# Kernel optimization log

Hardware: AMD Instinct MI355X
Metric: run time of the kernel (lower is better)

The kernel has to match this reference:

```python
import jax, jax.numpy as jnp
import numpy as np

EPS = 1e-3  # norm_cfg eps
# (kind, stride, padding) per conv; 'subm' = SubMConv3d (same spatial shape, same active mask),
# 'down' = SparseConv3d (strided, mask dilates through the kernel footprint)
_CFGS = [("subm", (1, 1, 1), (1, 1, 1)), ("subm", (1, 1, 1), (1, 1, 1)),
         ("down", (2, 2, 2), (1, 1, 1)), ("subm", (1, 1, 1), (1, 1, 1)),
         ("down", (2, 2, 2), (1, 1, 1)), ("subm", (1, 1, 1), (1, 1, 1)),
         ("down", (2, 2, 2), (1, 1, 0)), ("subm", (1, 1, 1), (1, 1, 1)),
         ("down", (1, 1, 2), (0, 0, 0))]
_WSHAPES = [(16, 16, 3, 3, 3), (16, 16, 3, 3, 3), (32, 16, 3, 3, 3), (32, 32, 3, 3, 3),
            (64, 32, 3, 3, 3), (64, 64, 3, 3, 3), (64, 64, 3, 3, 3), (64, 64, 3, 3, 3),
            (64, 64, 1, 1, 3)]


def _conv3d(x, w, stride, pad):
    return jax.lax.conv_general_dilated(
        x, w, window_strides=stride, padding=[(p, p) for p in pad],
        dimension_numbers=("NCDHW", "OIDHW", "NCDHW"))


def _bn_relu(x, mask, gamma, beta):
    # spconv applies BatchNorm1d to the [n_active, C] feature list, so batch statistics
    # are computed over ACTIVE voxels only; inactive sites stay exactly zero.
    cnt = jnp.maximum(mask.sum(), 1.0)
    mean = (x * mask).sum(axis=(0, 2, 3, 4)) / cnt
    mb = mean[None, :, None, None, None]
    var = (jnp.square(x - mb) * mask).sum(axis=(0, 2, 3, 4)) / cnt
    scale = (gamma * jax.lax.rsqrt(var + EPS))[None, :, None, None, None]
    y = (x - mb) * scale + beta[None, :, None, None, None]
    return jax.nn.relu(y) * mask


def _forward(voxel_features, coors, batch_size, input_shape, ws, gs, bs):
    ss = np.array(list(input_shape)[::-1]) + np.array([0, 0, 1])  # sparse_shape [D,H,W]
    D, H, W = int(ss[0]), int(ss[1]), int(ss[2])
    B, C = int(batch_size), voxel_features.shape[1]
    b, z, y, xi = coors[:, 0], coors[:, 1], coors[:, 2], coors[:, 3]
    # Densify: sparse conv with bias=False on a densified grid computes identical values
    # (inactive inputs are zero); the active-site mask reproduces submanifold masking and
    # the active-only BN statistics.
    x = jnp.zeros((B, C, D, H, W), voxel_features.dtype).at[b, :, z, y, xi].set(voxel_features)
    mask = jnp.zeros((B, 1, D, H, W), voxel_features.dtype).at[b, 0, z, y, xi].set(1.0)
    for (kind, stride, pad), w, g, be in zip(_CFGS, ws, gs, bs):
        x = _conv3d(x, w, stride, pad)
        if kind == "down":
            ones = jnp.ones((1, 1) + w.shape[2:], x.dtype)
            mask = (_conv3d(mask, ones, stride, pad) > 0).astype(x.dtype)
        x = _bn_relu(x, mask, g, be)
    x = x.transpose(0, 1, 4, 2, 3)  # [N, C, W, D, H]
    N, C2, Wd, Dd, Hd = x.shape
    return x.reshape(N, C2 * Wd, Dd, Hd)


def setup_inputs():
    rng = np.random.default_rng(0)
    D, H, W, n_vox, c_in = 40, 200, 200, 60000, 16
    lin = rng.choice(D * H * W, size=n_vox, replace=False)  # unique voxel coords
    coors = np.stack([np.zeros(n_vox, np.int32), (lin // (H * W)).astype(np.int32),
                      ((lin // W) % H).astype(np.int32), (lin % W).astype(np.int32)], axis=1)
    key = jax.random.key(0)
    keys = jax.random.split(key, 1 + len(_WSHAPES))
    out = {"voxel_features": jax.random.normal(keys[0], (n_vox, c_in), jnp.float32),
           "coors": jnp.asarray(coors), "batch_size": 1, "input_shape": (199, 200, 40)}
    for i, shp in enumerate(_WSHAPES):
        fan_in = shp[1] * shp[2] * shp[3] * shp[4]
        out[f"w{i}"] = jax.random.normal(keys[1 + i], shp, jnp.float32) / np.sqrt(fan_in)
        out[f"g{i}"] = jnp.ones((shp[0],), jnp.float32)
        out[f"b{i}"] = jnp.zeros((shp[0],), jnp.float32)
    return out


def reference(voxel_features, coors, batch_size, input_shape,
              w0, w1, w2, w3, w4, w5, w6, w7, w8,
              g0, g1, g2, g3, g4, g5, g6, g7, g8,
              b0, b1, b2, b3, b4, b5, b6, b7, b8):
    ws = [w0, w1, w2, w3, w4, w5, w6, w7, w8]
    gs = [g0, g1, g2, g3, g4, g5, g6, g7, g8]
    bs = [b0, b1, b2, b3, b4, b5, b6, b7, b8]
    return _forward(voxel_features, coors, batch_size, input_shape, ws, gs, bs)
```

## Files before the change

kernel.cpp:

```cpp
#include <hip/hip_runtime.h>
#include <cstddef>

#define EPSV 0.001f

static inline int idiv(int a, int b){ return (a + b - 1) / b; }
static inline int imin(int a, int b){ return a < b ? a : b; }

typedef __attribute__((ext_vector_type(8))) short short8b;
typedef __attribute__((ext_vector_type(4))) float floatx4;

static __device__ inline unsigned short f2bf(float f) {
  unsigned u = __float_as_uint(f);
  unsigned r = (u + 0x7FFFu + ((u >> 16) & 1u)) >> 16;
  return (unsigned short)r;
}

struct WPtrs { const float* w[9]; };

__global__ __launch_bounds__(256)
void repack_w(WPtrs ws, float* __restrict__ wp) {
  constexpr int off[10] = {0,6912,13824,27648,55296,110592,221184,331776,442368,454656};
  constexpr int COs[9] = {16,16,32,32,64,64,64,64,64};
  constexpr int CIs[9] = {16,16,16,32,32,64,64,64,64};
  constexpr int NTs[9] = {27,27,27,27,27,27,27,27,3};
  int idx = blockIdx.x * blockDim.x + threadIdx.x;
  if (idx >= off[9]) return;
  int L = 0;
  #pragma unroll
  for (int k = 0; k < 9; k++) if (idx >= off[k+1]) L = k + 1;
  int r  = idx - off[L];
  int CO = COs[L], CI = CIs[L], NT = NTs[L];
  int co = r % CO; int t = r / CO; int ci = t % CI; int tap = t / CI;
  wp[idx] = ws.w[L][(co*CI + ci)*NT + tap];
}

__global__ __launch_bounds__(256)
void repack_wq(const float* __restrict__ w6, const float* __restrict__ w7,
               const float* __restrict__ w8, float* __restrict__ wq) {
  constexpr int N6 = 110592, N7 = 110592, N8 = 12288;
  int idx = blockIdx.x * blockDim.x + threadIdx.x;
  if (idx >= N6 + N7 + N8) return;
  const float* src; int r; int NT;
  if (idx < N6)            { src = w6; r = idx;          NT = 27; }
  else if (idx < N6 + N7)  { src = w7; r = idx - N6;     NT = 27; }
  else                     { src = w8; r = idx - N6 - N7; NT = 3; }
  int j = r & 3; int co = (r >> 2) & 63; int chunk = (r >> 8) & 15; int tap = r >> 12;
  int ci = chunk*4 + j;
  wq[idx] = src[(co*64 + ci)*NT + tap];
}

__global__ __launch_bounds__(256)
void repack_w3b(const float* __restrict__ w3, unsigned short* __restrict__ wq3) {
  int idx = blockIdx.x * blockDim.x + threadIdx.x;
  if (idx >= 27648) return;
  int ci = idx % 32; int t = idx / 32; int co = t % 32; int tap = t / 32;
  wq3[idx] = f2bf(w3[(co*32 + ci)*27 + tap]);
}

__global__ __launch_bounds__(256)
void scatter_grid(const int* __restrict__ coors, int* __restrict__ grid, int n) {
  int i = blockIdx.x * blockDim.x + threadIdx.x;
  if (i >= n) return;
  int z = coors[4*i+1], y = coors[4*i+2], x = coors[4*i+3];
  grid[(z*200 + y)*200 + x] = i;
}

__global__ __launch_bounds__(256)
void subm16(const float* __restrict__ fin, float* __restrict__ fout,
            const int* __restrict__ coors, const int* __restrict__ grid,
            const float* __restrict__ wp, int n) {
  int i = blockIdx.x * blockDim.x + threadIdx.x;
  if (i >= n) return;
  int z = coors[4*i+1], y = coors[4*i+2], x = coors[4*i+3];
  float acc[16];
  #pragma unroll
  for (int c = 0; c < 16; c++) acc[c] = 0.f;
  for (int kz = 0; kz < 3; kz++) {
    int iz = z + kz - 1; if ((unsigned)iz >= 40u) continue;
    for (int ky = 0; ky < 3; ky++) {
      int iy = y + ky - 1; if ((unsigned)iy >= 200u) continue;
      for (int kx = 0; kx < 3; kx++) {
        int ix = x + kx - 1; if ((unsigned)ix >= 200u) continue;
        int j = grid[(iz*200 + iy)*200 + ix];
        if (j < 0) continue;
        int tap = (kz*3 + ky)*3 + kx;
        const float* fj = fin + (size_t)j*16;
        const float* wb = wp + tap*16*16;
        #pragma unroll
        for (int cq = 0; cq < 4; cq++) {
          float4 av = *reinterpret_cast<const float4*>(fj + cq*4);
          float aj[4] = {av.x, av.y, av.z, av.w};
          #pragma unroll
          for (int j4 = 0; j4 < 4; j4++) {
            #pragma unroll
            for (int c = 0; c < 16; c++) acc[c] += aj[j4] * wb[(cq*4+j4)*16 + c];
          }
        }
      }
    }
  }
  float* o = fout + (size_t)i*16;
  #pragma unroll
  for (int c = 0; c < 16; c++) o[c] = acc[c];
}

__global__ __launch_bounds__(256)
void down16to32(const float* __restrict__ fin, const int* __restrict__ grid,
                float* __restrict__ out, unsigned char* __restrict__ mout,
                const float* __restrict__ wp) {
  constexpr int OD = 20, OH = 100, OW = 100, COPT = 16;
  int vox = blockIdx.x * blockDim.x + threadIdx.x;
  int cog = blockIdx.y;
  if (vox >= OD*OH*OW) return;
  int ox = vox % OW; int t = vox / OW; int oy = t % OH; int oz = t / OH;
  float acc[COPT];
  #pragma unroll
  for (int c = 0; c < COPT; c++) acc[c] = 0.f;
  bool any = false;
  for (int kz = 0; kz < 3; kz++) {
    int iz = oz*2 - 1 + kz; if ((unsigned)iz >= 40u) continue;
    for (int ky = 0; ky < 3; ky++) {
      int iy = oy*2 - 1 + ky; if ((unsigned)iy >= 200u) continue;
      for (int kx = 0; kx < 3; kx++) {
        int ix = ox*2 - 1 + kx; if ((unsigned)ix >= 200u) continue;
        int j = grid[(iz*200 + iy)*200 + ix];
        if (j < 0) continue;
        any = true;
        int tap = (kz*3 + ky)*3 + kx;
        const float* fj = fin + (size_t)j*16;
        const float* wb = wp + (size_t)tap*16*32 + cog*COPT;
        #pragma unroll
        for (int cq = 0; cq < 4; cq++) {
          float4 av = *reinterpret_cast<const float4*>(fj + cq*4);
          float aj[4] = {av.x, av.y, av.z, av.w};
          #pragma unroll
          for (int j4 = 0; j4 < 4; j4++) {
            #pragma unroll
            for (int c = 0; c < COPT; c++) acc[c] += aj[j4] * wb[(cq*4+j4)*32 + c];
          }
        }
      }
    }
  }
  float* o = out + (size_t)vox*32 + cog*COPT;
  #pragma unroll
  for (int c = 0; c < COPT; c++) o[c] = acc[c];
  if (cog == 0) mout[vox] = any ? 1 : 0;
}

__global__ __launch_bounds__(256)
void convm3(const unsigned short* __restrict__ xb, float* __restrict__ out,
            const unsigned short* __restrict__ wq3) {
  constexpr int D = 20, H = 100, W = 100;
  constexpr int LDA = 40;
  __shared__ unsigned short a_lds[64 * LDA];
  __shared__ unsigned short w_lds[32 * LDA];

  const int tid  = threadIdx.x;
  const int lane = tid & 63;
  const int wv   = tid >> 6;
  const int vbase = blockIdx.x * 64;

  const int svox = tid >> 2, sq = tid & 3;
  int gv = vbase + svox;
  int sx = gv % W; int tt = gv / W; int sy = tt % H; int sz = tt / H;

  floatx4 acc0 = {0.f,0.f,0.f,0.f};
  floatx4 acc1 = {0.f,0.f,0.f,0.f};
  const int arow = wv*16 + (lane & 15);
  const int kc   = (lane >> 4) * 8;

  #pragma unroll 1
  for (int tap = 0; tap < 27; tap++) {
    int kz = tap / 9, r9 = tap % 9;
    int ky = r9 / 3, kx = r9 % 3;
    int iz = sz + kz - 1, iy = sy + ky - 1, ix = sx + kx - 1;
    bool ok = ((unsigned)iz < (unsigned)D) & ((unsigned)iy < (unsigned)H)
            & ((unsigned)ix < (unsigned)W);
    float4 av = make_float4(0.f,0.f,0.f,0.f);
    if (ok)
      av = *reinterpret_cast<const float4*>(
          xb + ((size_t)((iz*H + iy)*W + ix)*32 + sq*8));
    __syncthreads();
    *reinterpret_cast<float4*>(&a_lds[svox*LDA + sq*8]) = av;
    if (tid < 128) {
      int co = tid >> 2, h = tid & 3;
      *reinterpret_cast<float4*>(&w_lds[co*LDA + h*8]) =
          *reinterpret_cast<const float4*>(wq3 + ((size_t)(tap*32 + co)*32 + h*8));
    }
    __syncthreads();
    short8b a  = *reinterpret_cast<const short8b*>(&a_lds[arow*LDA + kc]);
    short8b b0 = *reinterpret_cast<const short8b*>(&w_lds[(lane & 15)*LDA + kc]);
    short8b b1 = *reinterpret_cast<const short8b*>(&w_lds[(16 + (lane & 15))*LDA + kc]);
    acc0 = __builtin_amdgcn_mfma_f32_16x16x32_bf16(a, b0, acc0, 0, 0, 0);
    acc1 = __builtin_amdgcn_mfma_f32_16x16x32_bf16(a, b1, acc1, 0, 0, 0);
  }
  int orow = vbase + wv*16 + (lane >> 4) * 4;
  int ocol = lane & 15;
  #pragma unroll
  for (int rr = 0; rr < 4; rr++) {
    out[(size_t)(orow + rr)*32 + ocol]      = acc0[rr];
    out[(size_t)(orow + rr)*32 + 16 + ocol] = acc1[rr];
  }
}

template<int ID,int IH,int IW,int OD,int OH,int OW,int CI,int CO,
         int S,int VX,int CO2,
         int KD,int KH,int KW,int SD,int SH,int SW,int PD,int PH,int PW>
__global__ __launch_bounds__(256)
void convg(const float* __restrict__ in, float* __restrict__ out,
           const float* __restrict__ wp) {
  constexpr int G    = 256 / S;
  static_assert(G * CO2 == CO, "co tiling mismatch");
  constexpr int VT   = S * VX;
  constexpr int NVOX = OD*OH*OW;
  __shared__ float a_lds[VT * CI];
  __shared__ float w_lds[CI * CO];

  const int g   = threadIdx.x % G;
  const int s   = threadIdx.x / G;
  const int co0 = g * CO2;
  const int vbase = blockIdx.x * VT;

  float acc[VX][CO2];
  #pragma unroll
  for (int u = 0; u < VX; u++)
    #pragma unroll
    for (int cc = 0; cc < CO2; cc++) acc[u][cc] = 0.f;

  constexpr int CI4N = CI / 4;
  constexpr int VST  = 256 / CI4N;
  const int sv  = threadIdx.x / CI4N;
  const int sc4 = threadIdx.x % CI4N;

  #pragma unroll 1
  for (int kz = 0; kz < KD; kz++) {
    #pragma unroll 1
    for (int ky = 0; ky < KH; ky++) {
      #pragma unroll 1
      for (int kx = 0; kx < KW; kx++) {
        __syncthreads();
        const float* wt = wp + (size_t)((kz*KH + ky)*KW + kx) * CI * CO;
        #pragma unroll
        for (int i = 0; i < CI*CO/4/256; i++) {
          int idx = threadIdx.x + i*256;
          *reinterpret_cast<float4*>(&w_lds[idx*4]) =
              *reinterpret_cast<const float4*>(wt + idx*4);
        }
        #pragma unroll
        for (int rsub = 0; rsub < VT/VST; rsub++) {
          int vox = rsub*VST + sv;
          int gv  = vbase + vox;
          int vc  = gv < NVOX ? gv : 0;
          int ox = vc % OW; int tt = vc / OW; int oy = tt % OH; int oz = tt / OH;
          int iz = oz*SD - PD + kz;
          int iy = oy*SH - PH + ky;
          int ix = ox*SW - PW + kx;
          bool ok = (gv < NVOX) & ((unsigned)iz < (unsigned)ID)
                  & ((unsigned)iy < (unsigned)IH) & ((unsigned)ix < (unsigned)IW);
          float4 v = make_float4(0.f,0.f,0.f,0.f);
          if (ok) {
            int ipos = (iz*IH + iy)*IW + ix;
            v = *reinterpret_cast<const float4*>(in + (size_t)ipos*CI + sc4*4);
          }
          int dw = vox*CI + ((sc4*4) ^ ((vox & 7) << 2));
          *reinterpret_cast<float4*>(&a_lds[dw]) = v;
        }
        __syncthreads();
        #pragma unroll
        for (int c4 = 0; c4 < CI/4; c4++) {
          float wr[4][CO2];
          #pragma unroll
          for (int jj = 0; jj < 4; jj++)
            #pragma unroll
            for (int q = 0; q < CO2/4; q++) {
              float4 wv = *reinterpret_cast<const float4*>(
                  &w_lds[(c4*4 + jj)*CO + co0 + q*4]);
              wr[jj][q*4+0] = wv.x; wr[jj][q*4+1] = wv.y;
              wr[jj][q*4+2] = wv.z; wr[jj][q*4+3] = wv.w;
            }
          #pragma unroll
          for (int u = 0; u < VX; u++) {
            int r = s + S*u;
            float4 a4 = *reinterpret_cast<const float4*>(
                &a_lds[r*CI + ((c4*4) ^ ((r & 7) << 2))]);
            float av[4] = {a4.x, a4.y, a4.z, a4.w};
            #pragma unroll
            for (int jj = 0; jj < 4; jj++)
              #pragma unroll
              for (int cc = 0; cc < CO2; cc++)
                acc[u][cc] += av[jj] * wr[jj][cc];
          }
        }
      }
    }
  }
  #pragma unroll
  for (int u = 0; u < VX; u++) {
    int gv = vbase + s + S*u;
    if (gv >= NVOX) continue;
    float* o = out + (size_t)gv*CO + co0;
    #pragma unroll
    for (int q = 0; q < CO2/4; q++) {
      float4 v = make_float4(acc[u][q*4+0], acc[u][q*4+1],
                             acc[u][q*4+2], acc[u][q*4+3]);
      *reinterpret_cast<float4*>(o + q*4) = v;
    }
  }
}

template<int ID,int IH,int IW,int OD,int OH,int OW,
         int KD,int KH,int KW,int SD,int SH,int SW,int PD,int PH,int PW>
__global__ __launch_bounds__(256)
void convt(const float* __restrict__ in, float* __restrict__ out,
           const float* __restrict__ wq) {
  constexpr int NT = KD*KH*KW;
  constexpr int NG = (NT + 3) / 4;
  const int v    = blockIdx.x;
  const int lane = threadIdx.x & 63;
  const int q    = threadIdx.x >> 6;
  int ox = v % OW; int t = v / OW; int oy = t % OH; int oz = t / OH;

  __shared__ float a_lds[4][64];
  __shared__ float red[4][64];
  float acc = 0.f;

  #pragma unroll 1
  for (int tg = 0; tg < NG; tg++) {
    int tap = tg*4 + q;
    float val = 0.f;
    if (tap < NT) {
      int kz = tap / (KH*KW); int rr = tap % (KH*KW);
      int ky = rr / KW;       int kx = rr % KW;
      int iz = oz*SD - PD + kz, iy = oy*SH - PH + ky, ix = ox*SW - PW + kx;
      if ((unsigned)iz < (unsigned)ID && (unsigned)iy < (unsigned)IH &&
          (unsigned)ix < (unsigned)IW)
        val = in[(size_t)((iz*IH + iy)*IW + ix)*64 + lane];
    }
    __syncthreads();
    a_lds[q][lane] = val;
    __syncthreads();
    #pragma unroll
    for (int t4 = 0; t4 < 4; t4++) {
      int tap2 = tg*4 + t4;
      if (tap2 >= NT) break;
      #pragma unroll
      for (int c4 = 0; c4 < 4; c4++) {
        float4 w4 = *reinterpret_cast<const float4*>(
            wq + ((size_t)((tap2*16 + q*4 + c4)*64 + lane) * 4));
        acc += w4.x * a_lds[t4][q*16 + c4*4 + 0];
        acc += w4.y * a_lds[t4][q*16 + c4*4 + 1];
        acc += w4.z * a_lds[t4][q*16 + c4*4 + 2];
        acc += w4.w * a_lds[t4][q*16 + c4*4 + 3];
      }
    }
  }
  red[q][lane] = acc;
  __syncthreads();
  if (q == 0) {
    float s = red[0][lane] + red[1][lane] + red[2][lane] + red[3][lane];
    out[(size_t)v*64 + lane] = s;
  }
}

template<int ID,int IH,int IW,int OD,int OH,int OW,int KD,int KH,int KW,
         int SD,int SH,int SW,int PD,int PH,int PW>
__global__ __launch_bounds__(256)
void mask_down(const unsigned char* __restrict__ min_, unsigned char* __restrict__ mout) {
  int v = blockIdx.x * blockDim.x + threadIdx.x;
  if (v >= OD*OH*OW) return;
  int ox = v % OW; int t = v / OW; int oy = t % OH; int oz = t / OH;
  bool any = false;
  for (int kz = 0; kz < KD; kz++) {
    int iz = oz*SD - PD + kz; if ((unsigned)iz >= (unsigned)ID) continue;
    for (int ky = 0; ky < KH; ky++) {
      int iy = oy*SH - PH + ky; if ((unsigned)iy >= (unsigned)IH) continue;
      for (int kx = 0; kx < KW; kx++) {
        int ix = ox*SW - PW + kx; if ((unsigned)ix >= (unsigned)IW) continue;
        any = any || (min_[(iz*IH + iy)*IW + ix] != 0);
      }
    }
  }
  mout[v] = any ? 1 : 0;
}

template<int CO, int YD>
__global__ void bn_stats(const float* __restrict__ x, const unsigned char* __restrict__ m,
                         float* __restrict__ stats, int nvox) {
  int c  = threadIdx.x;
  int ty = threadIdx.y;
  float s = 0.f, q = 0.f, cnt = 0.f;
  for (int vox = blockIdx.x*YD + ty; vox < nvox; vox += gridDim.x*YD) {
    bool act = m ? (m[vox] != 0) : true;
    if (act) {
      float v = x[(size_t)vox*CO + c];
      s += v; q += v*v; cnt += 1.f;
    }
  }
  __shared__ float ls[YD][CO];
  __shared__ float lq[YD][CO];
  __shared__ float lc[YD];
  ls[ty][c] = s; lq[ty][c] = q;
  if (c == 0) lc[ty] = cnt;
  __syncthreads();
  if (ty == 0) {
    #pragma unroll
    for (int i = 1; i < YD; i++) { s += ls[i][c]; q += lq[i][c]; }
    atomicAdd(&stats[c], s);
    atomicAdd(&stats[CO + c], q);
    if (c == 0) {
      float tc = 0.f;
      #pragma unroll
      for (int i = 0; i < YD; i++) tc += lc[i];
      atomicAdd(&stats[2*CO], tc);
    }
  }
}

template<int CO>
__global__ __launch_bounds__(256)
void bn_apply(float* __restrict__ x, const unsigned char* __restrict__ m,
              const float* __restrict__ stats, const float* __restrict__ g,
              const float* __restrict__ b, int nvox) {
  int idx = blockIdx.x * blockDim.x + threadIdx.x;
  int vox = idx / CO, c = idx % CO;
  if (vox >= nvox) return;
  float cnt   = fmaxf(stats[2*CO], 1.f);
  float mean  = stats[c] / cnt;
  float var   = stats[CO + c] / cnt - mean*mean;
  float scale = g[c] * rsqrtf(var + EPSV);
  float v = (x[idx] - mean) * scale + b[c];
  v = fmaxf(v, 0.f);
  bool act = m ? (m[vox] != 0) : true;
  x[idx] = act ? v : 0.f;
}

template<int CO>
__global__ __launch_bounds__(256)
void bn_apply_bf(float* __restrict__ x, const unsigned char* __restrict__ m,
                 const float* __restrict__ stats, const float* __restrict__ g,
                 const float* __restrict__ b, unsigned short* __restrict__ xb,
                 int nvox) {
  int idx = blockIdx.x * blockDim.x + threadIdx.x;
  int vox = idx / CO, c = idx % CO;
  if (vox >= nvox) return;
  float cnt   = fmaxf(stats[2*CO], 1.f);
  float mean  = stats[c] / cnt;
  float var   = stats[CO + c] / cnt - mean*mean;
  float scale = g[c] * rsqrtf(var + EPSV);
  float v = (x[idx] - mean) * scale + b[c];
  v = fmaxf(v, 0.f);
  bool act = m ? (m[vox] != 0) : true;
  v = act ? v : 0.f;
  x[idx]  = v;
  xb[idx] = f2bf(v);
}

__global__ __launch_bounds__(256)
void write_out(const float* __restrict__ x, float* __restrict__ out) {
  int idx = blockIdx.x * blockDim.x + threadIdx.x;
  if (idx >= 64*11*5*25) return;
  int y = idx % 25; int t = idx / 25;
  int z = t % 5;  t /= 5;
  int wx = t % 11; int c = t / 11;
  out[idx] = x[(((z*25 + y)*11) + wx)*64 + c];
}

extern "C" void kernel_launch(void* const* d_in, const int* in_sizes, int n_in,
                              void* d_out, int out_size, void* d_ws, size_t ws_size,
                              hipStream_t stream) {
  const float* vf    = (const float*)d_in[0];
  const int*   coors = (const int*)d_in[1];
  int n = in_sizes[0] / 16;

  const float *w[9], *g[9], *b[9];
  for (int i = 0; i < 9; i++) {
    w[i] = (const float*)d_in[4 + 3*i];
    g[i] = (const float*)d_in[5 + 3*i];
    b[i] = (const float*)d_in[6 + 3*i];
  }
  float* out = (float*)d_out;

  char* wsb = (char*)d_ws;
  size_t off = 0;
  auto alloc = [&](size_t bytes) -> void* {
    void* p = wsb + off;
    off += (bytes + 255) & ~(size_t)255;
    return p;
  };
  int*   grid0 = (int*)  alloc((size_t)40*200*200*4);
  float* fA    = (float*)alloc((size_t)n*16*4);
  float* fB    = (float*)alloc((size_t)n*16*4);
  float* wp    = (float*)alloc((size_t)454656*4);
  float* wq    = (float*)alloc((size_t)233472*4);
  unsigned short* wq3 = (unsigned short*)alloc((size_t)27648*2);
  float* dA    = (float*)alloc((size_t)20*100*100*32*4);
  float* dB    = (float*)alloc((size_t)20*100*100*32*4);
  unsigned char* m2 = (unsigned char*)alloc(20*100*100);
  unsigned char* m4 = (unsigned char*)alloc(10*50*50);
  unsigned char* m6 = (unsigned char*)alloc(5*25*24);
  unsigned char* m8 = (unsigned char*)alloc(5*25*11);
  float* stats = (float*)alloc((size_t)9*160*4);
  unsigned short* xB = (unsigned short*)grid0;

  float* st[9];
  for (int i = 0; i < 9; i++) st[i] = stats + i*160;

  hipMemsetAsync(grid0, 0xFF, (size_t)40*200*200*4, stream);
  hipMemsetAsync(stats, 0, (size_t)9*160*4, stream);

  WPtrs wps; for (int i = 0; i < 9; i++) wps.w[i] = w[i];
  repack_w<<<idiv(454656,256), 256, 0, stream>>>(wps, wp);
  repack_wq<<<idiv(233472,256), 256, 0, stream>>>(w[6], w[7], w[8], wq);
  repack_w3b<<<idiv(27648,256), 256, 0, stream>>>(w[3], wq3);
  scatter_grid<<<idiv(n,256), 256, 0, stream>>>(coors, grid0, n);

  const int WO0=0, WO1=6912, WO2=13824, WO4=55296, WO5=110592;
  const int WQ6=0, WQ7=110592, WQ8=221184;

  subm16<<<idiv(n,256), 256, 0, stream>>>(vf, fA, coors, grid0, wp + WO0, n);
  bn_stats<16,16><<<imin(256, idiv(n,16)), dim3(16,16), 0, stream>>>(fA, nullptr, st[0], n);
  bn_apply<16><<<idiv(n*16,256), 256, 0, stream>>>(fA, nullptr, st[0], g[0], b[0], n);

  subm16<<<idiv(n,256), 256, 0, stream>>>(fA, fB, coors, grid0, wp + WO1, n);
  bn_stats<16,16><<<imin(256, idiv(n,16)), dim3(16,16), 0, stream>>>(fB, nullptr, st[1], n);
  bn_apply<16><<<idiv(n*16,256), 256, 0, stream>>>(fB, nullptr, st[1], g[1], b[1], n);

  down16to32<<<dim3(idiv(200000,256),2), 256, 0, stream>>>(fB, grid0, dA, m2, wp + WO2);
  bn_stats<32,8><<<imin(256, idiv(200000,8)), dim3(32,8), 0, stream>>>(dA, m2, st[2], 200000);
  bn_apply_bf<32><<<idiv(200000*32,256), 256, 0, stream>>>(dA, m2, st[2], g[2], b[2], xB, 200000);

  convm3<<<200000/64, 256, 0, stream>>>(xB, dB, wq3);
  bn_stats<32,8><<<imin(256, idiv(200000,8)), dim3(32,8), 0, stream>>>(dB, m2, st[3], 200000);
  bn_apply<32><<<idiv(200000*32,256), 256, 0, stream>>>(dB, m2, st[3], g[3], b[3], 200000);

  convg<20,100,100, 10,50,50, 32,64, 16,4,4, 3,3,3, 2,2,2, 1,1,1>
      <<<idiv(25000,64), 256, 0, stream>>>(dB, dA, wp + WO4);
  mask_down<20,100,100, 10,50,50, 3,3,3, 2,2,2, 1,1,1>
      <<<idiv(25000,256), 256, 0, stream>>>(m2, m4);
  bn_stats<64,4><<<imin(256, idiv(25000,4)), dim3(64,4), 0, stream>>>(dA, m4, st[4], 25000);
  bn_apply<64><<<idiv(25000*64,256), 256, 0, stream>>>(dA, m4, st[4], g[4], b[4], 25000);

  convg<10,50,50, 10,50,50, 64,64, 16,4,4, 3,3,3, 1,1,1, 1,1,1>
      <<<idiv(25000,64), 256, 0, stream>>>(dA, dB, wp + WO5);
  bn_stats<64,4><<<imin(256, idiv(25000,4)), dim3(64,4), 0, stream>>>(dB, m4, st[5], 25000);
  bn_apply<64><<<idiv(25000*64,256), 256, 0, stream>>>(dB, m4, st[5], g[5], b[5], 25000);

  convt<10,50,50, 5,25,24, 3,3,3, 2,2,2, 1,1,0>
      <<<3000, 256, 0, stream>>>(dB, dA, wq + WQ6);
  mask_down<10,50,50, 5,25,24, 3,3,3, 2,2,2, 1,1,0>
      <<<idiv(3000,256), 256, 0, stream>>>(m4, m6);
  bn_stats<64,4><<<imin(256, idiv(3000,4)), dim3(64,4), 0, stream>>>(dA, m6, st[6], 3000);
  bn_apply<64><<<idiv(3000*64,256), 256, 0, stream>>>(dA, m6, st[6], g[6], b[6], 3000);

  convt<5,25,24, 5,25,24, 3,3,3, 1,1,1, 1,1,1>
      <<<3000, 256, 0, stream>>>(dA, dB, wq + WQ7);
  bn_stats<64,4><<<imin(256, idiv(3000,4)), dim3(64,4), 0, stream>>>(dB, m6, st[7], 3000);
  bn_apply<64><<<idiv(3000*64,256), 256, 0, stream>>>(dB, m6, st[7], g[7], b[7], 3000);

  convt<5,25,24, 5,25,11, 1,1,3, 1,1,2, 0,0,0>
      <<<1375, 256, 0, stream>>>(dB, dA, wq + WQ8);
  mask_down<5,25,24, 5,25,11, 1,1,3, 1,1,2, 0,0,0>
      <<<idiv(1375,256), 256, 0, stream>>>(m6, m8);
  bn_stats<64,4><<<imin(256, idiv(1375,4)), dim3(64,4), 0, stream>>>(dA, m8, st[8], 1375);
  bn_apply<64><<<idiv(1375*64,256), 256, 0, stream>>>(dA, m8, st[8], g[8], b[8], 1375);

  write_out<<<idiv(88000,256), 256, 0, stream>>>(dA, out);
}
```

Baseline: 816.8 us.

## Replace FP32 dense convs for layers 4-5 with bf16 MFMA implicit GEMM

Replaces the scalar FP32 convg kernel for conv layers 4 and 5 with a new convm kernel that runs an implicit GEMM on bf16 MFMA (16x16x32). The BN-apply steps feeding these layers now write bf16 activations, and new repack kernels convert the weights to bf16 in tap-major layout. The aim is to move the dominant conv FLOPs onto the matrix cores and halve input bandwidth, at the cost of reduced precision in activations and weights.

```diff
diff --git a/kernel.cpp b/kernel.cpp
--- a/kernel.cpp
+++ b/kernel.cpp
@@ -55,6 +55,20 @@
   if (idx >= 27648) return;
   int ci = idx % 32; int t = idx / 32; int co = t % 32; int tap = t / 32;
   wq3[idx] = f2bf(w3[(co*32 + ci)*27 + tap]);
+}
+
+__global__ __launch_bounds__(256)
+void repack_wmb(const float* __restrict__ w4, const float* __restrict__ w5,
+                unsigned short* __restrict__ q4, unsigned short* __restrict__ q5) {
+  int idx = blockIdx.x * blockDim.x + threadIdx.x;
+  if (idx < 55296) {
+    int ci = idx % 32; int t = idx / 32; int co = t % 64; int tap = t / 64;
+    q4[idx] = f2bf(w4[(co*32 + ci)*27 + tap]);
+  } else if (idx < 55296 + 110592) {
+    int r = idx - 55296;
+    int ci = r % 64; int t = r / 64; int co = t % 64; int tap = t / 64;
+    q5[r] = f2bf(w5[(co*64 + ci)*27 + tap]);
+  }
 }
 
 __global__ __launch_bounds__(256)
@@ -204,107 +218,100 @@
   }
 }
 
-template<int ID,int IH,int IW,int OD,int OH,int OW,int CI,int CO,
-         int S,int VX,int CO2,
-         int KD,int KH,int KW,int SD,int SH,int SW,int PD,int PH,int PW>
-__global__ __launch_bounds__(256)
-void convg(const float* __restrict__ in, float* __restrict__ out,
-           const float* __restrict__ wp) {
-  constexpr int G    = 256 / S;
-  static_assert(G * CO2 == CO, "co tiling mismatch");
-  constexpr int VT   = S * VX;
-  constexpr int NVOX = OD*OH*OW;
-  __shared__ float a_lds[VT * CI];
-  __shared__ float w_lds[CI * CO];
-
-  const int g   = threadIdx.x % G;
-  const int s   = threadIdx.x / G;
-  const int co0 = g * CO2;
-  const int vbase = blockIdx.x * VT;
-
-  float acc[VX][CO2];
-  #pragma unroll
-  for (int u = 0; u < VX; u++)
-    #pragma unroll
-    for (int cc = 0; cc < CO2; cc++) acc[u][cc] = 0.f;
-
-  constexpr int CI4N = CI / 4;
-  constexpr int VST  = 256 / CI4N;
-  const int sv  = threadIdx.x / CI4N;
-  const int sc4 = threadIdx.x % CI4N;
+template<int ID,int IH,int IW,int OD,int OH,int OW,int CI,
+         int SD,int SH,int SW,int PD,int PH,int PW>
+__global__ __launch_bounds__(256)
+void convm(const unsigned short* __restrict__ xb, float* __restrict__ out,
+           const unsigned short* __restrict__ wb) {
+  constexpr int CO  = 64;
+  constexpr int NVO = OD*OH*OW;
+  constexpr int LDA = CI + 8;
+  constexpr int NCH = CI / 32;
+  constexpr int CPR = CI / 8;
+  constexpr int AROWS = 256 / CPR;
+  constexpr int APASS = 64 / AROWS;
+  constexpr int WPASS = CO / AROWS;
+  __shared__ unsigned short a_lds[64 * LDA];
+  __shared__ unsigned short w_lds[CO * LDA];
+
+  const int tid  = threadIdx.x;
+  const int lane = tid & 63;
+  const int wv   = tid >> 6;
+  const int vbase = blockIdx.x * 64;
+
+  const int sva = tid / CPR;
+  const int sqa = tid % CPR;
+
+  floatx4 acc0 = {0.f,0.f,0.f,0.f};
+  floatx4 acc1 = {0.f,0.f,0.f,0.f};
+  floatx4 acc2 = {0.f,0.f,0.f,0.f};
+  floatx4 acc3 = {0.f,0.f,0.f,0.f};
+  const int arow = wv*16 + (lane & 15);
+  const int kq   = (lane >> 4) * 8;
+
+  int sx[APASS], sy[APASS], sz[APASS]; bool sval[APASS];
+  #pragma unroll
+  for (int p = 0; p < APASS; p++) {
+    int row = p*AROWS + sva;
+    int gv  = vbase + row;
+    sval[p] = (gv < NVO);
+    int gvc = sval[p] ? gv : 0;
+    sx[p] = gvc % OW; int tt = gvc / OW; sy[p] = tt % OH; sz[p] = tt / OH;
+  }
 
   #pragma unroll 1
-  for (int kz = 0; kz < KD; kz++) {
-    #pragma unroll 1
-    for (int ky = 0; ky < KH; ky++) {
-      #pragma unroll 1
-      for (int kx = 0; kx < KW; kx++) {
-        __syncthreads();
-        const float* wt = wp + (size_t)((kz*KH + ky)*KW + kx) * CI * CO;
-        #pragma unroll
-        for (int i = 0; i < CI*CO/4/256; i++) {
-          int idx = threadIdx.x + i*256;
-          *reinterpret_cast<float4*>(&w_lds[idx*4]) =
-              *reinterpret_cast<const float4*>(wt + idx*4);
-        }
-        #pragma unroll
-        for (int rsub = 0; rsub < VT/VST; rsub++) {
-          int vox = rsub*VST + sv;
-          int gv  = vbase + vox;
-          int vc  = gv < NVOX ? gv : 0;
-          int ox = vc % OW; int tt = vc / OW; int oy = tt % OH; int oz = tt / OH;
-          int iz = oz*SD - PD + kz;
-          int iy = oy*SH - PH + ky;
-          int ix = ox*SW - PW + kx;
-          bool ok = (gv < NVOX) & ((unsigned)iz < (unsigned)ID)
-                  & ((unsigned)iy < (unsigned)IH) & ((unsigned)ix < (unsigned)IW);
-          float4 v = make_float4(0.f,0.f,0.f,0.f);
-          if (ok) {
-            int ipos = (iz*IH + iy)*IW + ix;
-            v = *reinterpret_cast<const float4*>(in + (size_t)ipos*CI + sc4*4);
-          }
-          int dw = vox*CI + ((sc4*4) ^ ((vox & 7) << 2));
-          *reinterpret_cast<float4*>(&a_lds[dw]) = v;
-        }
-        __syncthreads();
-        #pragma unroll
-        for (int c4 = 0; c4 < CI/4; c4++) {
-          float wr[4][CO2];
-          #pragma unroll
-          for (int jj = 0; jj < 4; jj++)
-            #pragma unroll
-            for (int q = 0; q < CO2/4; q++) {
-              float4 wv = *reinterpret_cast<const float4*>(
-                  &w_lds[(c4*4 + jj)*CO + co0 + q*4]);
-              wr[jj][q*4+0] = wv.x; wr[jj][q*4+1] = wv.y;
-              wr[jj][q*4+2] = wv.z; wr[jj][q*4+3] = wv.w;
-            }
-          #pragma unroll
-          for (int u = 0; u < VX; u++) {
-            int r = s + S*u;
-            float4 a4 = *reinterpret_cast<const float4*>(
-                &a_lds[r*CI + ((c4*4) ^ ((r & 7) << 2))]);
-            float av[4] = {a4.x, a4.y, a4.z, a4.w};
-            #pragma unroll
-            for (int jj = 0; jj < 4; jj++)
-              #pragma unroll
-              for (int cc = 0; cc < CO2; cc++)
-                acc[u][cc] += av[jj] * wr[jj][cc];
-          }
-        }
-      }
-    }
-  }
-  #pragma unroll
-  for (int u = 0; u < VX; u++) {
-    int gv = vbase + s + S*u;
-    if (gv >= NVOX) continue;
-    float* o = out + (size_t)gv*CO + co0;
-    #pragma unroll
-    for (int q = 0; q < CO2/4; q++) {
-      float4 v = make_float4(acc[u][q*4+0], acc[u][q*4+1],
-                             acc[u][q*4+2], acc[u][q*4+3]);
-      *reinterpret_cast<float4*>(o + q*4) = v;
+  for (int tap = 0; tap < 27; tap++) {
+    int kz = tap / 9, r9 = tap % 9;
+    int ky = r9 / 3, kx = r9 % 3;
+    float4 avr[APASS];
+    #pragma unroll
+    for (int p = 0; p < APASS; p++) {
+      int iz = sz[p]*SD - PD + kz, iy = sy[p]*SH - PH + ky, ix = sx[p]*SW - PW + kx;
+      bool ok = sval[p] & ((unsigned)iz < (unsigned)ID)
+              & ((unsigned)iy < (unsigned)IH) & ((unsigned)ix < (unsigned)IW);
+      avr[p] = make_float4(0.f,0.f,0.f,0.f);
+      if (ok)
+        avr[p] = *reinterpret_cast<const float4*>(
+            xb + ((size_t)((iz*IH + iy)*IW + ix)*CI + sqa*8));
+    }
+    float4 wvr[WPASS];
+    #pragma unroll
+    for (int p = 0; p < WPASS; p++) {
+      int row = p*AROWS + sva;
+      wvr[p] = *reinterpret_cast<const float4*>(
+          wb + ((size_t)(tap*CO + row)*CI + sqa*8));
+    }
+    __syncthreads();
+    #pragma unroll
+    for (int p = 0; p < APASS; p++)
+      *reinterpret_cast<float4*>(&a_lds[(p*AROWS + sva)*LDA + sqa*8]) = avr[p];
+    #pragma unroll
+    for (int p = 0; p < WPASS; p++)
+      *reinterpret_cast<float4*>(&w_lds[(p*AROWS + sva)*LDA + sqa*8]) = wvr[p];
+    __syncthreads();
+    #pragma unroll
+    for (int c = 0; c < NCH; c++) {
+      short8b a = *reinterpret_cast<const short8b*>(&a_lds[arow*LDA + c*32 + kq]);
+      short8b b0 = *reinterpret_cast<const short8b*>(&w_lds[( 0 + (lane&15))*LDA + c*32 + kq]);
+      short8b b1 = *reinterpret_cast<const short8b*>(&w_lds[(16 + (lane&15))*LDA + c*32 + kq]);
+      short8b b2 = *reinterpret_cast<const short8b*>(&w_lds[(32 + (lane&15))*LDA + c*32 + kq]);
+      short8b b3 = *reinterpret_cast<const short8b*>(&w_lds[(48 + (lane&15))*LDA + c*32 + kq]);
+      acc0 = __builtin_amdgcn_mfma_f32_16x16x32_bf16(a, b0, acc0, 0, 0, 0);
+      acc1 = __builtin_amdgcn_mfma_f32_16x16x32_bf16(a, b1, acc1, 0, 0, 0);
+      acc2 = __builtin_amdgcn_mfma_f32_16x16x32_bf16(a, b2, acc2, 0, 0, 0);
+      acc3 = __builtin_amdgcn_mfma_f32_16x16x32_bf16(a, b3, acc3, 0, 0, 0);
+    }
+  }
+  int orow = vbase + wv*16 + (lane >> 4) * 4;
+  int ocol = lane & 15;
+  #pragma unroll
+  for (int rr = 0; rr < 4; rr++) {
+    if (orow + rr < NVO) {
+      float* o = out + (size_t)(orow + rr)*CO;
+      o[ 0 + ocol] = acc0[rr];
+      o[16 + ocol] = acc1[rr];
+      o[32 + ocol] = acc2[rr];
+      o[48 + ocol] = acc3[rr];
     }
   }
 }
@@ -494,8 +501,11 @@
   float* wp    = (float*)alloc((size_t)454656*4);
   float* wq    = (float*)alloc((size_t)233472*4);
   unsigned short* wq3 = (unsigned short*)alloc((size_t)27648*2);
+  unsigned short* wq4 = (unsigned short*)alloc((size_t)55296*2);
+  unsigned short* wq5 = (unsigned short*)alloc((size_t)110592*2);
   float* dA    = (float*)alloc((size_t)20*100*100*32*4);
   float* dB    = (float*)alloc((size_t)20*100*100*32*4);
+  unsigned short* xB5 = (unsigned short*)alloc((size_t)25000*64*2);
   unsigned char* m2 = (unsigned char*)alloc(20*100*100);
   unsigned char* m4 = (unsigned char*)alloc(10*50*50);
   unsigned char* m6 = (unsigned char*)alloc(5*25*24);
@@ -513,9 +523,10 @@
   repack_w<<<idiv(454656,256), 256, 0, stream>>>(wps, wp);
   repack_wq<<<idiv(233472,256), 256, 0, stream>>>(w[6], w[7], w[8], wq);
   repack_w3b<<<idiv(27648,256), 256, 0, stream>>>(w[3], wq3);
+  repack_wmb<<<idiv(165888,256), 256, 0, stream>>>(w[4], w[5], wq4, wq5);
   scatter_grid<<<idiv(n,256), 256, 0, stream>>>(coors, grid0, n);
 
-  const int WO0=0, WO1=6912, WO2=13824, WO4=55296, WO5=110592;
+  const int WO0=0, WO1=6912, WO2=13824;
   const int WQ6=0, WQ7=110592, WQ8=221184;
 
   subm16<<<idiv(n,256), 256, 0, stream>>>(vf, fA, coors, grid0, wp + WO0, n);
@@ -532,17 +543,17 @@
 
   convm3<<<200000/64, 256, 0, stream>>>(xB, dB, wq3);
   bn_stats<32,8><<<imin(256, idiv(200000,8)), dim3(32,8), 0, stream>>>(dB, m2, st[3], 200000);
-  bn_apply<32><<<idiv(200000*32,256), 256, 0, stream>>>(dB, m2, st[3], g[3], b[3], 200000);
-
-  convg<20,100,100, 10,50,50, 32,64, 16,4,4, 3,3,3, 2,2,2, 1,1,1>
-      <<<idiv(25000,64), 256, 0, stream>>>(dB, dA, wp + WO4);
+  bn_apply_bf<32><<<idiv(200000*32,256), 256, 0, stream>>>(dB, m2, st[3], g[3], b[3], xB, 200000);
+
+  convm<20,100,100, 10,50,50, 32, 2,2,2, 1,1,1>
+      <<<idiv(25000,64), 256, 0, stream>>>(xB, dA, wq4);
   mask_down<20,100,100, 10,50,50, 3,3,3, 2,2,2, 1,1,1>
       <<<idiv(25000,256), 256, 0, stream>>>(m2, m4);
   bn_stats<64,4><<<imin(256, idiv(25000,4)), dim3(64,4), 0, stream>>>(dA, m4, st[4], 25000);
-  bn_apply<64><<<idiv(25000*64,256), 256, 0, stream>>>(dA, m4, st[4], g[4], b[4], 25000);
-
-  convg<10,50,50, 10,50,50, 64,64, 16,4,4, 3,3,3, 1,1,1, 1,1,1>
-      <<<idiv(25000,64), 256, 0, stream>>>(dA, dB, wp + WO5);
+  bn_apply_bf<64><<<idiv(25000*64,256), 256, 0, stream>>>(dA, m4, st[4], g[4], b[4], xB5, 25000);
+
+  convm<10,50,50, 10,50,50, 64, 1,1,1, 1,1,1>
+      <<<idiv(25000,64), 256, 0, stream>>>(xB5, dB, wq5);
   bn_stats<64,4><<<imin(256, idiv(25000,4)), dim3(64,4), 0, stream>>>(dB, m4, st[5], 25000);
   bn_apply<64><<<idiv(25000*64,256), 256, 0, stream>>>(dB, m4, st[5], g[5], b[5], 25000);
 
```

New measurement: 710.9 us. -13.0%, faster.
